# Performance work log

Measured on AMD Instinct MI355X. Metric: run time of the kernel, lower is better.

The kernel has to match this reference:

```python
import jax, jax.numpy as jnp
import numpy as np

C = 1024
FACTOR = 4
C_INT = C * FACTOR


def setup_inputs() -> dict:
    key = jax.random.key(0)
    ks = jax.random.split(key, 6)
    act = jax.random.normal(ks[0], (4, 2048, C), dtype=jnp.float32)
    mask = jnp.ones((4, 2048), dtype=jnp.float32)
    # LayerNorm params
    ln_scale = jnp.ones((C,), dtype=jnp.float32)
    ln_bias = jnp.zeros((C,), dtype=jnp.float32)
    # Linear 1 (init='linear'): lecun-normal-ish
    w1 = jax.random.normal(ks[1], (C, C_INT), dtype=jnp.float32) / np.sqrt(C)
    b1 = jnp.zeros((C_INT,), dtype=jnp.float32)
    # Linear 2 (init='final' -> zeros in AF2; use small random so grads are nontrivial)
    w2 = jax.random.normal(ks[2], (C_INT, C), dtype=jnp.float32) * 0.02
    b2 = jnp.zeros((C,), dtype=jnp.float32)
    return {"act": act, "mask": mask, "ln_scale": ln_scale, "ln_bias": ln_bias,
            "w1": w1, "b1": b1, "w2": w2, "b2": b2}


def _layernorm(x, scale, bias, eps=1e-5):
    mu = jnp.mean(x, axis=-1, keepdims=True)
    var = jnp.mean(jnp.square(x - mu), axis=-1, keepdims=True)
    return (x - mu) * jax.lax.rsqrt(var + eps) * scale + bias


def reference(act, mask, ln_scale, ln_bias, w1, b1, w2, b2):
    # mask is accepted but unused, matching the original forward.
    x = _layernorm(act, ln_scale, ln_bias)
    h = jax.nn.relu(jnp.einsum('bsc,cf->bsf', x, w1) + b1)
    return jnp.einsum('bsf,fc->bsc', h, w2) + b2
```

## Files before the change

kernel.cpp:

```cpp
#include <hip/hip_runtime.h>
#include <hip/hip_bf16.h>
#include <cstdint>

typedef unsigned short u16;
typedef __bf16 bf16x8 __attribute__((ext_vector_type(8)));
typedef float floatx4 __attribute__((ext_vector_type(4)));

#define AS1 __attribute__((address_space(1)))
#define AS3 __attribute__((address_space(3)))

static __device__ __forceinline__ u16 f2bf(float f) {
    union { float f; unsigned int u; } v; v.f = f;
    unsigned int u = v.u;
    return (u16)((u + 0x7FFFu + ((u >> 16) & 1u)) >> 16);
}

__device__ __forceinline__ void transpose_body(
    const float* __restrict__ in, u16* __restrict__ out,
    int R, int Ccols, int bx, int by, int tid, float (*tile)[33])
{
    const int tx = tid & 31;
    const int ty = tid >> 5;
    const int c0 = bx * 32;
    const int r0 = by * 32;
#pragma unroll
    for (int i = 0; i < 32; i += 8)
        tile[ty + i][tx] = in[(size_t)(r0 + ty + i) * Ccols + (c0 + tx)];
    __syncthreads();
#pragma unroll
    for (int i = 0; i < 32; i += 8)
        out[(size_t)(c0 + ty + i) * R + (r0 + tx)] = f2bf(tile[tx][ty + i]);
}

__global__ __launch_bounds__(256)
void prep(const float* __restrict__ w1, const float* __restrict__ w2,
          const float* __restrict__ act, const float* __restrict__ ln_scale,
          const float* __restrict__ ln_bias,
          u16* __restrict__ W1t, u16* __restrict__ W2t, u16* __restrict__ X)
{
    __shared__ float smem[32][33];
    const int id  = blockIdx.x;
    const int tid = threadIdx.x;

    if (id < 4096) {
        transpose_body(w1, W1t, 1024, 4096, id & 127, id >> 7, tid, smem);
        return;
    }
    if (id < 8192) {
        const int t = id - 4096;
        transpose_body(w2, W2t, 4096, 1024, t & 31, t >> 5, tid, smem);
        return;
    }
    const int row = id - 8192;
    const float4 v = ((const float4*)(act + (size_t)row * 1024))[tid];
    float s  = v.x + v.y + v.z + v.w;
    float ss = v.x * v.x + v.y * v.y + v.z * v.z + v.w * v.w;
#pragma unroll
    for (int off = 32; off > 0; off >>= 1) {
        s  += __shfl_xor(s, off, 64);
        ss += __shfl_xor(ss, off, 64);
    }
    float* red = &smem[0][0];
    const int wave = tid >> 6, lane = tid & 63;
    if (lane == 0) { red[wave] = s; red[4 + wave] = ss; }
    __syncthreads();
    s  = red[0] + red[1] + red[2] + red[3];
    ss = red[4] + red[5] + red[6] + red[7];
    const float mu  = s * (1.0f / 1024.0f);
    const float var = ss * (1.0f / 1024.0f) - mu * mu;
    const float rs  = rsqrtf(var + 1e-5f);
    const float4 sc = ((const float4*)ln_scale)[tid];
    const float4 bi = ((const float4*)ln_bias)[tid];
    ushort4 o;
    o.x = f2bf((v.x - mu) * rs * sc.x + bi.x);
    o.y = f2bf((v.y - mu) * rs * sc.y + bi.y);
    o.z = f2bf((v.z - mu) * rs * sc.z + bi.z);
    o.w = f2bf((v.w - mu) * rs * sc.w + bi.w);
    ((ushort4*)(X + (size_t)row * 1024))[tid] = o;
}

template <int BK, bool BF16_OUT, bool RELU>
__global__ __launch_bounds__(256)
void gemm_bt(const u16* __restrict__ A,
             const u16* __restrict__ Bt,
             const float* __restrict__ bias,
             void* __restrict__ Cout,
             int M, int N, int K)
{
    constexpr int SLOTS  = BK / 8;
    constexpr int RPI    = 64 / SLOTS;
    constexpr int IPW    = SLOTS / 2;
    constexpr int HALVES = BK / 32;

    __shared__ __align__(16) u16 Alds[128 * BK];
    __shared__ __align__(16) u16 Blds[128 * BK];

    const int tid  = threadIdx.x;
    const int wave = tid >> 6;
    const int lane = tid & 63;
    const int wm   = wave & 1;
    const int wn   = wave >> 1;
    const int quad = lane >> 4;
    const int l16  = lane & 15;

    const int nbm = M >> 7;
    const int id  = blockIdx.x;
    const int bm  = id % nbm;
    const int bn  = id / nbm;

    const u16* Ag = A  + (size_t)bm * 128 * K;
    const u16* Bg = Bt + (size_t)bn * 128 * K;

    const int srow = lane / SLOTS;
    const int s_st = lane & (SLOTS - 1);

    const int rkey = (SLOTS == 4) ? ((l16 >> 1) & 3) : (l16 & (SLOTS - 1));

    floatx4 acc[4][4];
#pragma unroll
    for (int i = 0; i < 4; ++i)
#pragma unroll
        for (int j = 0; j < 4; ++j)
            acc[i][j] = (floatx4){0.f, 0.f, 0.f, 0.f};

    for (int k0 = 0; k0 < K; k0 += BK) {
        __syncthreads();
#pragma unroll
        for (int r = 0; r < IPW; ++r) {
            const int chunk = wave * IPW + r;
            const int row = chunk * RPI + srow;
            const int key = (SLOTS == 4) ? ((row >> 1) & 3)
                                         : (row & (SLOTS - 1));
            const int scol = (s_st ^ key) * 8;
            __builtin_amdgcn_global_load_lds(
                (AS1 void*)(Ag + (size_t)row * K + k0 + scol),
                (AS3 void*)(&Alds[chunk * 512]), 16, 0, 0);
            __builtin_amdgcn_global_load_lds(
                (AS1 void*)(Bg + (size_t)row * K + k0 + scol),
                (AS3 void*)(&Blds[chunk * 512]), 16, 0, 0);
        }
        __syncthreads();

#pragma unroll
        for (int h = 0; h < HALVES; ++h) {
            const int slot = ((quad + 4 * h) ^ rkey) * 8;
            bf16x8 bfr[4];
#pragma unroll
            for (int ni = 0; ni < 4; ++ni) {
                const int brow = wn * 64 + ni * 16 + l16;
                bfr[ni] = *(const bf16x8*)(&Blds[brow * BK + slot]);
            }
#pragma unroll
            for (int mi = 0; mi < 4; ++mi) {
                const int arow = wm * 64 + mi * 16 + l16;
                const bf16x8 a = *(const bf16x8*)(&Alds[arow * BK + slot]);
#pragma unroll
                for (int ni = 0; ni < 4; ++ni)
                    acc[mi][ni] = __builtin_amdgcn_mfma_f32_16x16x32_bf16(
                        bfr[ni], a, acc[mi][ni], 0, 0, 0);
            }
        }
    }

    const int mbase = bm * 128 + wm * 64;
    const int nbase = bn * 128 + wn * 64;
#pragma unroll
    for (int mi = 0; mi < 4; ++mi) {
        const int m = mbase + mi * 16 + l16;
#pragma unroll
        for (int ni = 0; ni < 4; ++ni) {
            const int n0 = nbase + ni * 16 + quad * 4;
            const float4 bv = *(const float4*)&bias[n0];
            float v0 = acc[mi][ni][0] + bv.x;
            float v1 = acc[mi][ni][1] + bv.y;
            float v2 = acc[mi][ni][2] + bv.z;
            float v3 = acc[mi][ni][3] + bv.w;
            if (RELU) {
                v0 = fmaxf(v0, 0.f); v1 = fmaxf(v1, 0.f);
                v2 = fmaxf(v2, 0.f); v3 = fmaxf(v3, 0.f);
            }
            if (BF16_OUT) {
                ushort4 o = { f2bf(v0), f2bf(v1), f2bf(v2), f2bf(v3) };
                *(ushort4*)&((u16*)Cout)[(size_t)m * N + n0] = o;
            } else {
                float4 o = { v0, v1, v2, v3 };
                *(float4*)&((float*)Cout)[(size_t)m * N + n0] = o;
            }
        }
    }
}

extern "C" void kernel_launch(void* const* d_in, const int* in_sizes, int n_in,
                              void* d_out, int out_size, void* d_ws, size_t ws_size,
                              hipStream_t stream)
{
    const float* act      = (const float*)d_in[0];
    const float* ln_scale = (const float*)d_in[2];
    const float* ln_bias  = (const float*)d_in[3];
    const float* w1       = (const float*)d_in[4];
    const float* b1       = (const float*)d_in[5];
    const float* w2       = (const float*)d_in[6];
    const float* b2       = (const float*)d_in[7];
    float* out = (float*)d_out;

    const int M = 8192, C = 1024, CI = 4096;

    u16* X   = (u16*)d_ws;
    u16* W1t = X   + (size_t)M * C;
    u16* W2t = W1t + (size_t)CI * C;
    u16* H   = W2t + (size_t)C * CI;

    prep<<<16384, 256, 0, stream>>>(w1, w2, act, ln_scale, ln_bias, W1t, W2t, X);
    gemm_bt<64, true, true><<<(M / 128) * (CI / 128), 256, 0, stream>>>(
        X, W1t, b1, (void*)H, M, CI, C);
    gemm_bt<128, false, false><<<(M / 128) * (C / 128), 256, 0, stream>>>(
        H, W2t, b2, (void*)out, M, C, CI);
}
```

Measured before the change: 268.0 us.

## Replace LDS-staged GEMMs with register-prefetched direct-load GEMMs and widen transposes

Both GEMMs stop staging tiles in LDS. Each wave now loads its MFMA fragments straight from global memory into registers, using a four-stage software pipeline that overlaps loads with MFMA work. Blocks grow to 512 threads covering 256x128 output tiles, and the K dimension becomes a template parameter. The weight transpose in prep is reworked to handle 128x32 tiles with float4 loads and ushort2 stores, cutting the prep grid size. The risk is losing LDS data reuse across waves, which adds redundant global/L2 traffic, and heavy register use from the prefetch buffers.

```diff
diff --git a/kernel.cpp b/kernel.cpp
--- a/kernel.cpp
+++ b/kernel.cpp
@@ -5,9 +5,6 @@
 typedef unsigned short u16;
 typedef __bf16 bf16x8 __attribute__((ext_vector_type(8)));
 typedef float floatx4 __attribute__((ext_vector_type(4)));
-
-#define AS1 __attribute__((address_space(1)))
-#define AS3 __attribute__((address_space(3)))
 
 static __device__ __forceinline__ u16 f2bf(float f) {
     union { float f; unsigned int u; } v; v.f = f;
@@ -19,17 +16,23 @@
     const float* __restrict__ in, u16* __restrict__ out,
     int R, int Ccols, int bx, int by, int tid, float (*tile)[33])
 {
-    const int tx = tid & 31;
-    const int ty = tid >> 5;
-    const int c0 = bx * 32;
-    const int r0 = by * 32;
-#pragma unroll
-    for (int i = 0; i < 32; i += 8)
-        tile[ty + i][tx] = in[(size_t)(r0 + ty + i) * Ccols + (c0 + tx)];
+    const int r0 = by * 128, c0 = bx * 32;
+#pragma unroll
+    for (int p = 0; p < 4; ++p) {
+        const int f = p * 256 + tid;
+        const int r = f >> 3, c4 = (f & 7) * 4;
+        const float4 v = *(const float4*)&in[(size_t)(r0 + r) * Ccols + c0 + c4];
+        tile[r][c4 + 0] = v.x; tile[r][c4 + 1] = v.y;
+        tile[r][c4 + 2] = v.z; tile[r][c4 + 3] = v.w;
+    }
     __syncthreads();
-#pragma unroll
-    for (int i = 0; i < 32; i += 8)
-        out[(size_t)(c0 + ty + i) * R + (r0 + tx)] = f2bf(tile[tx][ty + i]);
+    const int wv = tid >> 6, ln = tid & 63;
+#pragma unroll
+    for (int i = 0; i < 8; ++i) {
+        const int c = i * 4 + wv;
+        ushort2 o = { f2bf(tile[ln * 2][c]), f2bf(tile[ln * 2 + 1][c]) };
+        *(ushort2*)&out[(size_t)(c0 + c) * R + r0 + ln * 2] = o;
+    }
 }
 
 __global__ __launch_bounds__(256)
@@ -38,20 +41,20 @@
           const float* __restrict__ ln_bias,
           u16* __restrict__ W1t, u16* __restrict__ W2t, u16* __restrict__ X)
 {
-    __shared__ float smem[32][33];
+    __shared__ float tile[128][33];
     const int id  = blockIdx.x;
     const int tid = threadIdx.x;
 
-    if (id < 4096) {
-        transpose_body(w1, W1t, 1024, 4096, id & 127, id >> 7, tid, smem);
+    if (id < 1024) {
+        transpose_body(w1, W1t, 1024, 4096, id & 127, id >> 7, tid, tile);
         return;
     }
-    if (id < 8192) {
-        const int t = id - 4096;
-        transpose_body(w2, W2t, 4096, 1024, t & 31, t >> 5, tid, smem);
+    if (id < 2048) {
+        const int t = id - 1024;
+        transpose_body(w2, W2t, 4096, 1024, t & 31, t >> 5, tid, tile);
         return;
     }
-    const int row = id - 8192;
+    const int row = id - 2048;
     const float4 v = ((const float4*)(act + (size_t)row * 1024))[tid];
     float s  = v.x + v.y + v.z + v.w;
     float ss = v.x * v.x + v.y * v.y + v.z * v.z + v.w * v.w;
@@ -60,7 +63,7 @@
         s  += __shfl_xor(s, off, 64);
         ss += __shfl_xor(ss, off, 64);
     }
-    float* red = &smem[0][0];
+    float* red = &tile[0][0];
     const int wave = tid >> 6, lane = tid & 63;
     if (lane == 0) { red[wave] = s; red[4 + wave] = ss; }
     __syncthreads();
@@ -79,42 +82,52 @@
     ((ushort4*)(X + (size_t)row * 1024))[tid] = o;
 }
 
-template <int BK, bool BF16_OUT, bool RELU>
-__global__ __launch_bounds__(256)
-void gemm_bt(const u16* __restrict__ A,
-             const u16* __restrict__ Bt,
-             const float* __restrict__ bias,
-             void* __restrict__ Cout,
-             int M, int N, int K)
-{
-    constexpr int SLOTS  = BK / 8;
-    constexpr int RPI    = 64 / SLOTS;
-    constexpr int IPW    = SLOTS / 2;
-    constexpr int HALVES = BK / 32;
-
-    __shared__ __align__(16) u16 Alds[128 * BK];
-    __shared__ __align__(16) u16 Blds[128 * BK];
-
+#define LOADG(g, ks)                                                          \
+    do {                                                                      \
+        _Pragma("unroll")                                                     \
+        for (int mi = 0; mi < 4; ++mi)                                        \
+            fa##g[mi] = *(const bf16x8*)(Ap + (size_t)mi * 16 * K +           \
+                                         (size_t)(ks) * 32);                  \
+        _Pragma("unroll")                                                     \
+        for (int ni = 0; ni < 4; ++ni)                                        \
+            fb##g[ni] = *(const bf16x8*)(Bp + (size_t)ni * 16 * K +           \
+                                         (size_t)(ks) * 32);                  \
+    } while (0)
+
+#define MMAG(g)                                                               \
+    do {                                                                      \
+        _Pragma("unroll")                                                     \
+        for (int mi = 0; mi < 4; ++mi)                                        \
+            _Pragma("unroll")                                                 \
+            for (int ni = 0; ni < 4; ++ni)                                    \
+                acc[mi][ni] = __builtin_amdgcn_mfma_f32_16x16x32_bf16(        \
+                    fb##g[ni], fa##g[mi], acc[mi][ni], 0, 0, 0);              \
+    } while (0)
+
+template <int K, bool BF16_OUT, bool RELU>
+__global__ __launch_bounds__(512, 2)
+void gemm_reg(const u16* __restrict__ A, const u16* __restrict__ Bt,
+              const float* __restrict__ bias, void* __restrict__ Cout,
+              int M, int N)
+{
     const int tid  = threadIdx.x;
     const int wave = tid >> 6;
     const int lane = tid & 63;
-    const int wm   = wave & 1;
-    const int wn   = wave >> 1;
     const int quad = lane >> 4;
     const int l16  = lane & 15;
-
-    const int nbm = M >> 7;
+    const int wm   = wave >> 1;
+    const int wn   = wave & 1;
+
+    const int nbm = M >> 8;
     const int id  = blockIdx.x;
     const int bm  = id % nbm;
     const int bn  = id / nbm;
 
-    const u16* Ag = A  + (size_t)bm * 128 * K;
-    const u16* Bg = Bt + (size_t)bn * 128 * K;
-
-    const int srow = lane / SLOTS;
-    const int s_st = lane & (SLOTS - 1);
-
-    const int rkey = (SLOTS == 4) ? ((l16 >> 1) & 3) : (l16 & (SLOTS - 1));
+    const u16* Ap = A  + (size_t)(bm * 256 + wm * 64 + l16) * K + quad * 8;
+    const u16* Bp = Bt + (size_t)(bn * 128 + wn * 64 + l16) * K + quad * 8;
+
+    bf16x8 fa0[4], fb0[4], fa1[4], fb1[4];
+    bf16x8 fa2[4], fb2[4], fa3[4], fb3[4];
 
     floatx4 acc[4][4];
 #pragma unroll
@@ -123,46 +136,25 @@
         for (int j = 0; j < 4; ++j)
             acc[i][j] = (floatx4){0.f, 0.f, 0.f, 0.f};
 
-    for (int k0 = 0; k0 < K; k0 += BK) {
-        __syncthreads();
-#pragma unroll
-        for (int r = 0; r < IPW; ++r) {
-            const int chunk = wave * IPW + r;
-            const int row = chunk * RPI + srow;
-            const int key = (SLOTS == 4) ? ((row >> 1) & 3)
-                                         : (row & (SLOTS - 1));
-            const int scol = (s_st ^ key) * 8;
-            __builtin_amdgcn_global_load_lds(
-                (AS1 void*)(Ag + (size_t)row * K + k0 + scol),
-                (AS3 void*)(&Alds[chunk * 512]), 16, 0, 0);
-            __builtin_amdgcn_global_load_lds(
-                (AS1 void*)(Bg + (size_t)row * K + k0 + scol),
-                (AS3 void*)(&Blds[chunk * 512]), 16, 0, 0);
-        }
-        __syncthreads();
-
-#pragma unroll
-        for (int h = 0; h < HALVES; ++h) {
-            const int slot = ((quad + 4 * h) ^ rkey) * 8;
-            bf16x8 bfr[4];
-#pragma unroll
-            for (int ni = 0; ni < 4; ++ni) {
-                const int brow = wn * 64 + ni * 16 + l16;
-                bfr[ni] = *(const bf16x8*)(&Blds[brow * BK + slot]);
-            }
-#pragma unroll
-            for (int mi = 0; mi < 4; ++mi) {
-                const int arow = wm * 64 + mi * 16 + l16;
-                const bf16x8 a = *(const bf16x8*)(&Alds[arow * BK + slot]);
-#pragma unroll
-                for (int ni = 0; ni < 4; ++ni)
-                    acc[mi][ni] = __builtin_amdgcn_mfma_f32_16x16x32_bf16(
-                        bfr[ni], a, acc[mi][ni], 0, 0, 0);
-            }
-        }
-    }
-
-    const int mbase = bm * 128 + wm * 64;
+    constexpr int NT = K / 32;
+    constexpr int NI = NT / 4;
+
+    LOADG(0, 0);
+    LOADG(1, 1);
+
+    for (int i = 0; i < NI - 1; ++i) {
+        const int b = 4 * i;
+        LOADG(2, b + 2); MMAG(0);
+        LOADG(3, b + 3); MMAG(1);
+        LOADG(0, b + 4); MMAG(2);
+        LOADG(1, b + 5); MMAG(3);
+    }
+    LOADG(2, NT - 2); MMAG(0);
+    LOADG(3, NT - 1); MMAG(1);
+    MMAG(2);
+    MMAG(3);
+
+    const int mbase = bm * 256 + wm * 64;
     const int nbase = bn * 128 + wn * 64;
 #pragma unroll
     for (int mi = 0; mi < 4; ++mi) {
@@ -210,9 +202,9 @@
     u16* W2t = W1t + (size_t)CI * C;
     u16* H   = W2t + (size_t)C * CI;
 
-    prep<<<16384, 256, 0, stream>>>(w1, w2, act, ln_scale, ln_bias, W1t, W2t, X);
-    gemm_bt<64, true, true><<<(M / 128) * (CI / 128), 256, 0, stream>>>(
-        X, W1t, b1, (void*)H, M, CI, C);
-    gemm_bt<128, false, false><<<(M / 128) * (C / 128), 256, 0, stream>>>(
-        H, W2t, b2, (void*)out, M, C, CI);
-}
+    prep<<<10240, 256, 0, stream>>>(w1, w2, act, ln_scale, ln_bias, W1t, W2t, X);
+    gemm_reg<1024, true, true><<<(M / 256) * (CI / 128), 512, 0, stream>>>(
+        X, W1t, b1, (void*)H, M, CI);
+    gemm_reg<4096, false, false><<<(M / 256) * (C / 128), 512, 0, stream>>>(
+        H, W2t, b2, (void*)out, M, C);
+}
```

Measured after the change: 581.9 us. 117% more time.
